# Kernel tuning notes

Hardware: AMD Instinct MI355X
Metric: run time of the kernel (lower is better)

Reference implementation:

```python
import jax, jax.numpy as jnp
import numpy as np

EPS = 1e-18

_SOBEL_H = jnp.array([[-1., -2., -1.], [0., 0., 0.], [1., 2., 1.]], dtype=jnp.float32)


def _sobel_mag(x, eps):
    # x: [B,1,H,W]; depth-1 3x3 conv with 'same' padding, two fixed kernels
    wh = _SOBEL_H.reshape(1, 1, 3, 3).astype(x.dtype)   # horizontal kernel
    wv = _SOBEL_H.T.reshape(1, 1, 3, 3).astype(x.dtype)  # vertical kernel
    dn = jax.lax.conv_dimension_numbers(x.shape, wh.shape, ('NCHW', 'OIHW', 'NCHW'))
    gv = jax.lax.conv_general_dilated(x, wv, (1, 1), 'SAME', dimension_numbers=dn)
    gh = jax.lax.conv_general_dilated(x, wh, (1, 1), 'SAME', dimension_numbers=dn)
    return jnp.sqrt(gv * gv + gh * gh + eps)


def setup_inputs() -> dict:
    key = jax.random.key(0)
    k1, k2 = jax.random.split(key)
    shape = (64, 1, 512, 512)
    y_p = jax.random.uniform(k1, shape, dtype=jnp.float32)
    y_t = jax.random.uniform(k2, shape, dtype=jnp.float32)
    return {"y_p": y_p, "y_t": y_t}


def reference(y_p, y_t):
    eps = EPS
    ypg = _sobel_mag(y_p, eps)
    ytg = _sobel_mag(y_t, eps)
    out = (ytg - ypg) ** 2
    mask = (out == 0.0).astype(out.dtype)
    out = out + mask * eps
    out = jnp.sqrt(out + eps) * (1.0 - mask)
    return jnp.mean(out)
```

## Files before the change

kernel.cpp:

```cpp
#include <hip/hip_runtime.h>

#define IMG_W 512
#define IMG_H 512
#define BATCH 64
#define ROWS_PER_WAVE 8
#define WAVES_PER_BLOCK 4
#define ROWS_PER_BLOCK (ROWS_PER_WAVE * WAVES_PER_BLOCK)
#define SLABS (IMG_H / ROWS_PER_BLOCK)
#define NBLOCKS (BATCH * SLABS)
#define NPIX (BATCH * IMG_W * IMG_H)

__device__ __forceinline__ float fast_sqrtf(float x) {
    return __builtin_amdgcn_sqrtf(x);
}

__global__ __launch_bounds__(256) void sobel_loss_kernel(
    const float* __restrict__ yp, const float* __restrict__ yt,
    float* __restrict__ bsums)
{
    __shared__ float wred[WAVES_PER_BLOCK];

    const int tid  = threadIdx.x;
    const int lane = tid & 63;
    const int wv   = tid >> 6;
    const int bid  = blockIdx.x;
    const int b    = bid >> 4;
    const int slab = bid & (SLABS - 1);
    const int y0   = slab * ROWS_PER_BLOCK + wv * ROWS_PER_WAVE;
    const int x0   = lane << 3;

    const float* __restrict__ imgp = yp + (size_t)b * (IMG_W * IMG_H);
    const float* __restrict__ imgt = yt + (size_t)b * (IMG_W * IMG_H);

    float hp[3][10], ht[3][10];

    auto load_row = [&](int slot, int y) {
        float4 ap = {0.f, 0.f, 0.f, 0.f}, bp = {0.f, 0.f, 0.f, 0.f};
        float4 at = {0.f, 0.f, 0.f, 0.f}, bt = {0.f, 0.f, 0.f, 0.f};
        if (y >= 0 && y < IMG_H) {
            const float* rp = imgp + (size_t)y * IMG_W + x0;
            const float* rt = imgt + (size_t)y * IMG_W + x0;
            ap = *(const float4*)rp;
            bp = *(const float4*)(rp + 4);
            at = *(const float4*)rt;
            bt = *(const float4*)(rt + 4);
        }
        float lp  = __shfl_up(bp.w, 1, 64);
        float rp_ = __shfl_down(ap.x, 1, 64);
        float lt  = __shfl_up(bt.w, 1, 64);
        float rt_ = __shfl_down(at.x, 1, 64);
        if (lane == 0)  { lp = 0.f; lt = 0.f; }
        if (lane == 63) { rp_ = 0.f; rt_ = 0.f; }
        hp[slot][0] = lp;   ht[slot][0] = lt;
        hp[slot][1] = ap.x; hp[slot][2] = ap.y; hp[slot][3] = ap.z; hp[slot][4] = ap.w;
        hp[slot][5] = bp.x; hp[slot][6] = bp.y; hp[slot][7] = bp.z; hp[slot][8] = bp.w;
        ht[slot][1] = at.x; ht[slot][2] = at.y; ht[slot][3] = at.z; ht[slot][4] = at.w;
        ht[slot][5] = bt.x; ht[slot][6] = bt.y; ht[slot][7] = bt.z; ht[slot][8] = bt.w;
        hp[slot][9] = rp_;  ht[slot][9] = rt_;
    };

    float lsum = 0.f;

#define SOBEL_STEP(S0, S1, S2, YNEXT)                                          \
    do {                                                                       \
        load_row(S2, (YNEXT));                                                 \
        float cp[10], ct[10];                                                  \
        _Pragma("unroll")                                                      \
        for (int k = 0; k < 10; ++k) {                                         \
            cp[k] = fmaf(2.f, hp[S1][k], hp[S0][k]) + hp[S2][k];               \
            ct[k] = fmaf(2.f, ht[S1][k], ht[S0][k]) + ht[S2][k];               \
        }                                                                      \
        _Pragma("unroll")                                                      \
        for (int j = 0; j < 8; ++j) {                                          \
            float tp  = fmaf(2.f, hp[S2][j + 1], hp[S2][j]) + hp[S2][j + 2];   \
            float bp_ = fmaf(2.f, hp[S0][j + 1], hp[S0][j]) + hp[S0][j + 2];   \
            float ghp = tp - bp_;                                              \
            float gvp = cp[j + 2] - cp[j];                                     \
            float magp = fast_sqrtf(fmaf(gvp, gvp, fmaf(ghp, ghp, 1e-18f)));   \
            float tt  = fmaf(2.f, ht[S2][j + 1], ht[S2][j]) + ht[S2][j + 2];   \
            float bt_ = fmaf(2.f, ht[S0][j + 1], ht[S0][j]) + ht[S0][j + 2];   \
            float ght = tt - bt_;                                              \
            float gvt = ct[j + 2] - ct[j];                                     \
            float magt = fast_sqrtf(fmaf(gvt, gvt, fmaf(ght, ght, 1e-18f)));   \
            lsum += fabsf(magt - magp);         \
        }                                                                      \
    } while (0)

    load_row(0, y0 - 1);
    load_row(1, y0);
    SOBEL_STEP(0, 1, 2, y0 + 1);
    SOBEL_STEP(1, 2, 0, y0 + 2);
    SOBEL_STEP(2, 0, 1, y0 + 3);
    SOBEL_STEP(0, 1, 2, y0 + 4);
    SOBEL_STEP(1, 2, 0, y0 + 5);
    SOBEL_STEP(2, 0, 1, y0 + 6);
    SOBEL_STEP(0, 1, 2, y0 + 7);
    SOBEL_STEP(1, 2, 0, y0 + 8);
#undef SOBEL_STEP

#pragma unroll
    for (int off = 32; off > 0; off >>= 1)
        lsum += __shfl_down(lsum, off, 64);
    if (lane == 0) wred[wv] = lsum;
    __syncthreads();
    if (tid == 0)
        bsums[bid] = wred[0] + wred[1] + wred[2] + wred[3];
}

__global__ __launch_bounds__(256) void reduce_final(
    const float* __restrict__ bsums, float* __restrict__ out)
{
    __shared__ float wred[4];
    const int tid = threadIdx.x;
    float s = 0.f;
    for (int i = tid; i < NBLOCKS; i += 256) s += bsums[i];
#pragma unroll
    for (int off = 32; off > 0; off >>= 1)
        s += __shfl_down(s, off, 64);
    if ((tid & 63) == 0) wred[tid >> 6] = s;
    __syncthreads();
    if (tid == 0)
        out[0] = (wred[0] + wred[1] + wred[2] + wred[3]) * (1.0f / (float)NPIX);
}

extern "C" void kernel_launch(void* const* d_in, const int* in_sizes, int n_in,
                              void* d_out, int out_size, void* d_ws, size_t ws_size,
                              hipStream_t stream) {
    const float* yp = (const float*)d_in[0];
    const float* yt = (const float*)d_in[1];
    float* out = (float*)d_out;

    float* bsums = (float*)d_ws;
    sobel_loss_kernel<<<NBLOCKS, 256, 0, stream>>>(yp, yt, bsums);
    reduce_final<<<1, 256, 0, stream>>>(bsums, out);
}
```

Baseline: 151.0 us.

## Use single-wave blocks and software-pipeline row loads two rows ahead

Each block becomes a single 64-lane wave handling 8 rows, which removes the shared-memory reduction and __syncthreads and quadruples the block count. Row loads are issued two rows ahead into double-buffered float4 registers and assembled into the halo arrays later, so global loads overlap the Sobel arithmetic. This raises register pressure, can lower occupancy, and sends four times as many partial sums to the final reduction.

Result: no change. 150.1 us (-0.6%).

```diff
diff --git a/kernel.cpp b/kernel.cpp
--- a/kernel.cpp
+++ b/kernel.cpp
@@ -4,9 +4,7 @@
 #define IMG_H 512
 #define BATCH 64
 #define ROWS_PER_WAVE 8
-#define WAVES_PER_BLOCK 4
-#define ROWS_PER_BLOCK (ROWS_PER_WAVE * WAVES_PER_BLOCK)
-#define SLABS (IMG_H / ROWS_PER_BLOCK)
+#define SLABS (IMG_H / ROWS_PER_WAVE)
 #define NBLOCKS (BATCH * SLABS)
 #define NPIX (BATCH * IMG_W * IMG_H)
 
@@ -14,56 +12,64 @@
     return __builtin_amdgcn_sqrtf(x);
 }
 
-__global__ __launch_bounds__(256) void sobel_loss_kernel(
+__global__ __launch_bounds__(64) void sobel_loss_kernel(
     const float* __restrict__ yp, const float* __restrict__ yt,
     float* __restrict__ bsums)
 {
-    __shared__ float wred[WAVES_PER_BLOCK];
-
-    const int tid  = threadIdx.x;
-    const int lane = tid & 63;
-    const int wv   = tid >> 6;
+    const int lane = threadIdx.x;
     const int bid  = blockIdx.x;
-    const int b    = bid >> 4;
+    const int b    = bid >> 6;
     const int slab = bid & (SLABS - 1);
-    const int y0   = slab * ROWS_PER_BLOCK + wv * ROWS_PER_WAVE;
+    const int y0   = slab * ROWS_PER_WAVE;
     const int x0   = lane << 3;
 
     const float* __restrict__ imgp = yp + (size_t)b * (IMG_W * IMG_H);
     const float* __restrict__ imgt = yt + (size_t)b * (IMG_W * IMG_H);
 
     float hp[3][10], ht[3][10];
+    float4 A0p, B0p, A0t, B0t;
+    float4 A1p, B1p, A1t, B1t;
 
-    auto load_row = [&](int slot, int y) {
-        float4 ap = {0.f, 0.f, 0.f, 0.f}, bp = {0.f, 0.f, 0.f, 0.f};
-        float4 at = {0.f, 0.f, 0.f, 0.f}, bt = {0.f, 0.f, 0.f, 0.f};
-        if (y >= 0 && y < IMG_H) {
-            const float* rp = imgp + (size_t)y * IMG_W + x0;
-            const float* rt = imgt + (size_t)y * IMG_W + x0;
-            ap = *(const float4*)rp;
-            bp = *(const float4*)(rp + 4);
-            at = *(const float4*)rt;
-            bt = *(const float4*)(rt + 4);
-        }
-        float lp  = __shfl_up(bp.w, 1, 64);
-        float rp_ = __shfl_down(ap.x, 1, 64);
-        float lt  = __shfl_up(bt.w, 1, 64);
-        float rt_ = __shfl_down(at.x, 1, 64);
-        if (lane == 0)  { lp = 0.f; lt = 0.f; }
-        if (lane == 63) { rp_ = 0.f; rt_ = 0.f; }
-        hp[slot][0] = lp;   ht[slot][0] = lt;
-        hp[slot][1] = ap.x; hp[slot][2] = ap.y; hp[slot][3] = ap.z; hp[slot][4] = ap.w;
-        hp[slot][5] = bp.x; hp[slot][6] = bp.y; hp[slot][7] = bp.z; hp[slot][8] = bp.w;
-        ht[slot][1] = at.x; ht[slot][2] = at.y; ht[slot][3] = at.z; ht[slot][4] = at.w;
-        ht[slot][5] = bt.x; ht[slot][6] = bt.y; ht[slot][7] = bt.z; ht[slot][8] = bt.w;
-        hp[slot][9] = rp_;  ht[slot][9] = rt_;
-    };
+#define ISSUE(S, Y)                                                            \
+    do {                                                                       \
+        int yy = (Y);                                                          \
+        if (yy >= 0 && yy < IMG_H) {                                           \
+            const float* rp = imgp + (size_t)yy * IMG_W + x0;                  \
+            const float* rt = imgt + (size_t)yy * IMG_W + x0;                  \
+            A##S##p = *(const float4*)rp;                                      \
+            B##S##p = *(const float4*)(rp + 4);                                \
+            A##S##t = *(const float4*)rt;                                      \
+            B##S##t = *(const float4*)(rt + 4);                                \
+        } else {                                                               \
+            A##S##p = {0.f, 0.f, 0.f, 0.f}; B##S##p = {0.f, 0.f, 0.f, 0.f};   \
+            A##S##t = {0.f, 0.f, 0.f, 0.f}; B##S##t = {0.f, 0.f, 0.f, 0.f};   \
+        }                                                                      \
+    } while (0)
+
+#define ASSEMBLE(S, R)                                                         \
+    do {                                                                       \
+        float lp  = __shfl_up(B##S##p.w, 1, 64);                               \
+        float rp_ = __shfl_down(A##S##p.x, 1, 64);                             \
+        float lt  = __shfl_up(B##S##t.w, 1, 64);                               \
+        float rt_ = __shfl_down(A##S##t.x, 1, 64);                             \
+        if (lane == 0)  { lp = 0.f; lt = 0.f; }                                \
+        if (lane == 63) { rp_ = 0.f; rt_ = 0.f; }                              \
+        hp[R][0] = lp;      ht[R][0] = lt;                                     \
+        hp[R][1] = A##S##p.x; hp[R][2] = A##S##p.y;                            \
+        hp[R][3] = A##S##p.z; hp[R][4] = A##S##p.w;                            \
+        hp[R][5] = B##S##p.x; hp[R][6] = B##S##p.y;                            \
+        hp[R][7] = B##S##p.z; hp[R][8] = B##S##p.w;                            \
+        ht[R][1] = A##S##t.x; ht[R][2] = A##S##t.y;                            \
+        ht[R][3] = A##S##t.z; ht[R][4] = A##S##t.w;                            \
+        ht[R][5] = B##S##t.x; ht[R][6] = B##S##t.y;                            \
+        ht[R][7] = B##S##t.z; ht[R][8] = B##S##t.w;                            \
+        hp[R][9] = rp_;     ht[R][9] = rt_;                                    \
+    } while (0)
 
     float lsum = 0.f;
 
-#define SOBEL_STEP(S0, S1, S2, YNEXT)                                          \
+#define COMPUTE(S0, S1, S2)                                                    \
     do {                                                                       \
-        load_row(S2, (YNEXT));                                                 \
         float cp[10], ct[10];                                                  \
         _Pragma("unroll")                                                      \
         for (int k = 0; k < 10; ++k) {                                         \
@@ -86,25 +92,29 @@
         }                                                                      \
     } while (0)
 
-    load_row(0, y0 - 1);
-    load_row(1, y0);
-    SOBEL_STEP(0, 1, 2, y0 + 1);
-    SOBEL_STEP(1, 2, 0, y0 + 2);
-    SOBEL_STEP(2, 0, 1, y0 + 3);
-    SOBEL_STEP(0, 1, 2, y0 + 4);
-    SOBEL_STEP(1, 2, 0, y0 + 5);
-    SOBEL_STEP(2, 0, 1, y0 + 6);
-    SOBEL_STEP(0, 1, 2, y0 + 7);
-    SOBEL_STEP(1, 2, 0, y0 + 8);
-#undef SOBEL_STEP
+    ISSUE(0, y0 - 1);
+    ISSUE(1, y0);
+    ASSEMBLE(0, 0);  ISSUE(0, y0 + 1);
+    ASSEMBLE(1, 1);  ISSUE(1, y0 + 2);
+
+    ASSEMBLE(0, 2);  ISSUE(0, y0 + 3);  COMPUTE(0, 1, 2);
+    ASSEMBLE(1, 0);  ISSUE(1, y0 + 4);  COMPUTE(1, 2, 0);
+    ASSEMBLE(0, 1);  ISSUE(0, y0 + 5);  COMPUTE(2, 0, 1);
+    ASSEMBLE(1, 2);  ISSUE(1, y0 + 6);  COMPUTE(0, 1, 2);
+    ASSEMBLE(0, 0);  ISSUE(0, y0 + 7);  COMPUTE(1, 2, 0);
+    ASSEMBLE(1, 1);  ISSUE(1, y0 + 8);  COMPUTE(2, 0, 1);
+    ASSEMBLE(0, 2);                     COMPUTE(0, 1, 2);
+    ASSEMBLE(1, 0);                     COMPUTE(1, 2, 0);
+
+#undef ISSUE
+#undef ASSEMBLE
+#undef COMPUTE
 
 #pragma unroll
     for (int off = 32; off > 0; off >>= 1)
         lsum += __shfl_down(lsum, off, 64);
-    if (lane == 0) wred[wv] = lsum;
-    __syncthreads();
-    if (tid == 0)
-        bsums[bid] = wred[0] + wred[1] + wred[2] + wred[3];
+    if (lane == 0)
+        bsums[bid] = lsum;
 }
 
 __global__ __launch_bounds__(256) void reduce_final(
@@ -131,6 +141,6 @@
     float* out = (float*)d_out;
 
     float* bsums = (float*)d_ws;
-    sobel_loss_kernel<<<NBLOCKS, 256, 0, stream>>>(yp, yt, bsums);
+    sobel_loss_kernel<<<NBLOCKS, 64, 0, stream>>>(yp, yt, bsums);
     reduce_final<<<1, 256, 0, stream>>>(bsums, out);
 }
```
